# Performance work log

Measured on AMD Instinct MI355X. Metric: run time of the kernel, lower is better.

## Reference

```python
import jax, jax.numpy as jnp
import numpy as np

B, T, HID = 2, 1024, 768
EXPAND, NH, HD, NG, NS, K = 2, 24, 64, 1, 128, 4
INTER = EXPAND * HID            # 1536
CONV_DIM = INTER + 2 * NG * NS  # 1792
NLVL = 15                       # get_num_levels(16384, base=2)
EPS = 1e-5


def _levels(T):
    # Fenwick-style hierarchical level matrix (HType.WEAK, base 2):
    # level(t, s) = 0 on the diagonal, else msb(t XOR s) + 1.
    t = np.arange(T)
    x = t[:, None] ^ t[None, :]
    lev = np.zeros((T, T), np.int32)
    nz = x > 0
    lev[nz] = np.floor(np.log2(x[nz])).astype(np.int32) + 1
    return lev

_LEV = jnp.asarray(_levels(T))  # [T,T] int32, values in [0, NLVL)


def setup_inputs() -> dict:
    key = jax.random.key(0)
    ks = jax.random.split(key, 4)
    P = INTER + CONV_DIM + NH * (NLVL + 1)  # 3712
    return {
        "hidden_states": jax.random.normal(ks[0], (B, T, HID), jnp.float32),
        "in_proj_w": jax.random.normal(ks[1], (P, HID), jnp.float32) * (HID ** -0.5),
        "conv_w": jax.random.normal(ks[2], (CONV_DIM, 1, K), jnp.float32) * 0.2,
        "conv_b": jnp.zeros((CONV_DIM,), jnp.float32),
        "dt_bias": jnp.ones((NH,), jnp.float32),
        "A_log": jnp.log(jnp.arange(1, NH + 1, dtype=jnp.float32)),
        "L": jnp.ones((NH, NLVL), jnp.float32),
        "D": jnp.ones((NH,), jnp.float32),
        "norm_weight": jnp.ones((INTER,), jnp.float32),
        "out_proj_w": jax.random.normal(ks[3], (HID, INTER), jnp.float32) * (INTER ** -0.5),
    }


def reference(hidden_states, in_proj_w, conv_w, conv_b, dt_bias, A_log, L, D,
              norm_weight, out_proj_w):
    # in_proj and split: [gate | xBC | dt | dl]
    proj = hidden_states @ in_proj_w.T                       # [B,T,P]
    gate = proj[..., :INTER]
    xBC = proj[..., INTER:INTER + CONV_DIM]
    dt = proj[..., INTER + CONV_DIM:INTER + CONV_DIM + NH]
    dl = proj[..., INTER + CONV_DIM + NH:].reshape(B, T, NH, NLVL)

    # fused causal depthwise conv1d + SiLU
    xBC = jax.lax.conv_general_dilated(
        xBC.transpose(0, 2, 1), conv_w, window_strides=(1,),
        padding=[(K - 1, 0)], dimension_numbers=("NCH", "OIH", "NCH"),
        feature_group_count=CONV_DIM) + conv_b[None, :, None]
    xBC = jax.nn.silu(xBC.transpose(0, 2, 1))                # [B,T,CONV_DIM]

    x = xBC[..., :INTER].reshape(B, T, NH, HD)               # [B,T,H,P]
    Bm = xBC[..., INTER:INTER + NG * NS].reshape(B, T, NG, NS)
    Cm = xBC[..., INTER + NG * NS:].reshape(B, T, NG, NS)
    hpg = NH // NG
    Bh = jnp.repeat(Bm, hpg, axis=2)                         # [B,T,H,N]
    Ch = jnp.repeat(Cm, hpg, axis=2)

    dt = jax.nn.softplus(dt + dt_bias)                       # [B,T,H]
    A = -jnp.exp(A_log)                                      # [H]
    cumA = jnp.cumsum(dt * A, axis=1)                        # [B,T,H]

    # semiseparable decay exp(sum_{s<r<=t} dt_r * A), causal-masked
    cA = cumA.transpose(0, 2, 1)                             # [B,H,T]
    diff = cA[:, :, :, None] - cA[:, :, None, :]             # [B,H,T,T]
    mask = jnp.tril(jnp.ones((T, T), bool))
    decay = jnp.exp(jnp.where(mask[None, None], diff, -1e9))

    CB = jnp.einsum("bthn,bshn->bhts", Ch, Bh)               # [B,H,T,T]

    # hierarchical lambda gating: positive lambda, per-head learned scale L
    lam = jax.nn.softplus(dl) * L                            # [B,T,H,NLVL]
    lam_g = jnp.take_along_axis(lam.transpose(0, 2, 1, 3),
                                _LEV[None, None], axis=-1)   # [B,H,T,T]

    M = CB * decay * lam_g * dt.transpose(0, 2, 1)[:, :, None, :]
    y = jnp.einsum("bhts,bshp->bthp", M, x)                  # [B,T,H,P]
    y = y + D[None, None, :, None] * x
    y = y.reshape(B, T, INTER)

    # gated RMSNorm (norm_before_gate=False): norm(y * silu(gate))
    y = y * jax.nn.silu(gate)
    var = jnp.mean(jnp.square(y), axis=-1, keepdims=True)
    y = y * jax.lax.rsqrt(var + EPS) * norm_weight

    return y @ out_proj_w.T                                  # [B,T,HID]
```

## Files before the change

### kernel.cpp

```cpp
#include <hip/hip_runtime.h>
#include <hip/hip_bf16.h>
#include <math.h>

#define B_ 2
#define T_ 1024
#define HID_ 768
#define INTER_ 1536
#define NH_ 24
#define HD_ 64
#define NS_ 128
#define NLVL_ 15
#define CONV_DIM_ 1792
#define P_ 3712
#define EPS_ 1e-5f

typedef short short8_t __attribute__((ext_vector_type(8)));
typedef short short4_t __attribute__((ext_vector_type(4)));
typedef float float4_t __attribute__((ext_vector_type(4)));


__device__ __forceinline__ float softplus_f(float x) {
  return (x > 20.f) ? x : log1pf(__expf(x));
}
__device__ __forceinline__ short f2bf(float f) {
  union { float f; unsigned u; } v; v.f = f;
  unsigned r = v.u + 0x7FFF + ((v.u >> 16) & 1);
  return (short)(r >> 16);
}
__device__ __forceinline__ float bf2f(short s) {
  union { unsigned u; float f; } v; v.u = ((unsigned)(unsigned short)s) << 16;
  return v.f;
}
__device__ __forceinline__ void gl_lds16(const void* g, void* l) {
  __builtin_amdgcn_global_load_lds(
      (const __attribute__((address_space(1))) unsigned int*)g,
      (__attribute__((address_space(3))) unsigned int*)l, 16, 0, 0);
}

__global__ __launch_bounds__(256) void cvtdt_k(
    const float* __restrict__ hs, const float* __restrict__ Win, const float* __restrict__ Wout,
    short* __restrict__ hsbf, short* __restrict__ wibf, short* __restrict__ wobf,
    float* __restrict__ dtraw, int ncvt)
{
  const long na = (long)B_ * T_ * HID_, nb = (long)P_ * HID_, nc = (long)HID_ * INTER_;
  if ((int)blockIdx.x < ncvt) {
    const long i = ((long)blockIdx.x * 256 + threadIdx.x) * 8;
    const float* src; short* dst; long off;
    if (i < na)           { src = hs;   dst = hsbf; off = i; }
    else if (i < na + nb) { src = Win;  dst = wibf; off = i - na; }
    else if (i < na + nb + nc) { src = Wout; dst = wobf; off = i - na - nb; }
    else return;
    const long base = (off & ~31L) + ((off >> 3) & 3) * 4;
    float4 v0 = *(const float4*)(src + base);
    float4 v1 = *(const float4*)(src + base + 16);
    short8_t o;
    o[0] = f2bf(v0.x); o[1] = f2bf(v0.y); o[2] = f2bf(v0.z); o[3] = f2bf(v0.w);
    o[4] = f2bf(v1.x); o[5] = f2bf(v1.y); o[6] = f2bf(v1.z); o[7] = f2bf(v1.w);
    *(short8_t*)(dst + off) = o;
  } else {
    const int rowbt = ((int)blockIdx.x - ncvt) * 4 + (threadIdx.x >> 6);
    const int lane = threadIdx.x & 63;
    float hv[12];
    const float* hrow = hs + (long)rowbt * HID_ + lane * 12;
    #pragma unroll
    for (int j = 0; j < 12; j++) hv[j] = hrow[j];
    const float* wbase = Win + (long)(INTER_ + CONV_DIM_) * HID_ + lane * 12;
    for (int h = 0; h < NH_; h++) {
      const float* wr = wbase + (long)h * HID_;
      float s = 0.f;
      #pragma unroll
      for (int j = 0; j < 12; j++) s = fmaf(hv[j], wr[j], s);
      #pragma unroll
      for (int off = 32; off; off >>= 1) s += __shfl_xor(s, off);
      if (lane == 0) dtraw[(long)rowbt * NH_ + h] = s;
    }
  }
}

__device__ __forceinline__ short8_t ldfrag(const short* Ts, int row, int lg) {
  return *(const short8_t*)(Ts + row * 32 + lg * 8);
}

__device__ __forceinline__ short8_t ldfrag64(const short* Ts, int row, int kk, int lg) {
  const int cc = (kk * 4 + lg) ^ (row & 7);
  return *(const short8_t*)(Ts + row * 64 + cc * 8);
}

__global__ __launch_bounds__(256) void inproj_scan_k(
    const short* __restrict__ A, const short* __restrict__ B, short* __restrict__ C,
    const float* __restrict__ dtraw, const float* __restrict__ dt_bias,
    const float* __restrict__ A_log, float* __restrict__ dtT, float* __restrict__ cAT,
    float* __restrict__ qT)
{
  constexpr int TM = 128, TN = 128, K = HID_;
  constexpr int ASZ = TM * 32, BSZ = TN * 32;
  __shared__ short As[2 * ASZ];
  __shared__ short Bs[2 * BSZ];

  if (blockIdx.y >= 16) {
    const int sid = ((int)blockIdx.y - 16) * 29 + (int)blockIdx.x;
    if (sid >= B_ * NH_) return;
    const int b = sid / NH_;
    const int h = sid % NH_;
    const float bias = dt_bias[h];
    const float Ah = -__expf(A_log[h]);
    const long ob = (long)(h * B_ + b) * T_;
    float* sc = (float*)As;
    float carry = 0.f;
    for (int c0 = 0; c0 < T_; c0 += 256) {
      const int t = c0 + threadIdx.x;
      const long bt = (long)b * T_ + t;
      float sp = softplus_f(dtraw[bt * NH_ + h] + bias);
      dtT[ob + t] = sp;
      sc[threadIdx.x] = sp * Ah;
      __syncthreads();
      for (int off = 1; off < 256; off <<= 1) {
        float add = (threadIdx.x >= off) ? sc[threadIdx.x - off] : 0.f;
        __syncthreads();
        sc[threadIdx.x] += add;
        __syncthreads();
      }
      cAT[ob + t] = carry + sc[threadIdx.x];
      qT[ob + t] = sp * __expf(sc[threadIdx.x | 63] - sc[threadIdx.x]);
      float tot = sc[255];
      __syncthreads();
      carry += tot;
    }
    return;
  }

  const int tid = threadIdx.x;
  const int w = tid >> 6, lane = tid & 63;
  const int lr = lane & 15, lg = lane >> 4;
  const int wr = w >> 1, wc = w & 1;
  const int m0 = blockIdx.y * TM, n0 = blockIdx.x * TN;
  const int srow = lane >> 2;
  const int sc2 = (lane & 3) * 8;

  auto stage = [&](int buf, int k0) {
    #pragma unroll
    for (int it = 0; it < TM / 64; it++) {
      const int cb = w + 4 * it;
      const int row = cb * 16 + srow;
      gl_lds16(A + (long)(m0 + row) * K + k0 + sc2, As + buf * ASZ + cb * 512);
    }
    #pragma unroll
    for (int it = 0; it < TN / 64; it++) {
      const int cb = w + 4 * it;
      const int row = cb * 16 + srow;
      gl_lds16(B + (long)(n0 + row) * K + k0 + sc2, Bs + buf * BSZ + cb * 512);
    }
  };

  float4_t acc[4][4] = {};
  int cur = 0;
  stage(0, 0);
  for (int k0 = 0; k0 < K; k0 += 32) {
    __syncthreads();
    if (k0 + 32 < K) stage(cur ^ 1, k0 + 32);
    const short* Ab = As + cur * ASZ;
    const short* Bb = Bs + cur * BSZ;
    short8_t af[4], bf[4];
    #pragma unroll
    for (int m = 0; m < 4; m++) af[m] = ldfrag(Ab, wr * 64 + m * 16 + lr, lg);
    #pragma unroll
    for (int n = 0; n < 4; n++) bf[n] = ldfrag(Bb, wc * 64 + n * 16 + lr, lg);
    #pragma unroll
    for (int m = 0; m < 4; m++)
      #pragma unroll
      for (int n = 0; n < 4; n++)
        acc[m][n] = __builtin_amdgcn_mfma_f32_16x16x32_bf16(af[m], bf[n], acc[m][n], 0, 0, 0);
    cur ^= 1;
  }

  #pragma unroll
  for (int m = 0; m < 4; m++)
    #pragma unroll
    for (int n = 0; n < 4; n++)
      #pragma unroll
      for (int r = 0; r < 4; r++) {
        const int row = m0 + wr * 64 + m * 16 + lg * 4 + r;
        const int col = n0 + wc * 64 + n * 16 + lr;
        C[(long)row * P_ + col] = f2bf(acc[m][n][r]);
      }
}

__global__ __launch_bounds__(256) void gemm_out_k(
    const short* __restrict__ A, const short* __restrict__ B, float* __restrict__ C,
    int M, int N, int K)
{
  constexpr int PSZ = 64 * 32;
  constexpr int BKG = 4;
  constexpr int BUF = PSZ * BKG;
  __shared__ short As[2 * BUF];
  __shared__ short Bs[2 * BUF];
  const int tid = threadIdx.x;
  const int w = tid >> 6, lane = tid & 63;
  const int lr = lane & 15, lg = lane >> 4;
  const int wr = w >> 1, wc = w & 1;
  const int m0 = blockIdx.y * 64, n0 = blockIdx.x * 64;
  const int srow = lane >> 2;
  const int sc = (lane & 3) * 8;

  auto stage = [&](int buf, int k0) {
    const int row = w * 16 + srow;
    #pragma unroll
    for (int kg = 0; kg < BKG; kg++) {
      gl_lds16(A + (long)(m0 + row) * K + k0 + kg * 32 + sc, As + buf * BUF + kg * PSZ + w * 512);
      gl_lds16(B + (long)(n0 + row) * K + k0 + kg * 32 + sc, Bs + buf * BUF + kg * PSZ + w * 512);
    }
  };

  float4_t acc[2][2] = {};
  int cur = 0;
  stage(0, 0);
  for (int k0 = 0; k0 < K; k0 += 128) {
    __syncthreads();
    if (k0 + 128 < K) stage(cur ^ 1, k0 + 128);
    #pragma unroll
    for (int kg = 0; kg < BKG; kg++) {
      const short* Ab = As + cur * BUF + kg * PSZ;
      const short* Bb = Bs + cur * BUF + kg * PSZ;
      short8_t af[2], bf[2];
      #pragma unroll
      for (int m = 0; m < 2; m++) af[m] = ldfrag(Ab, wr * 32 + m * 16 + lr, lg);
      #pragma unroll
      for (int n = 0; n < 2; n++) bf[n] = ldfrag(Bb, wc * 32 + n * 16 + lr, lg);
      #pragma unroll
      for (int m = 0; m < 2; m++)
        #pragma unroll
        for (int n = 0; n < 2; n++)
          acc[m][n] = __builtin_amdgcn_mfma_f32_16x16x32_bf16(af[m], bf[n], acc[m][n], 0, 0, 0);
    }
    cur ^= 1;
  }

  #pragma unroll
  for (int m = 0; m < 2; m++)
    #pragma unroll
    for (int n = 0; n < 2; n++)
      #pragma unroll
      for (int r = 0; r < 4; r++) {
        const int row = m0 + wr * 32 + m * 16 + lg * 4 + r;
        const int col = n0 + wc * 32 + n * 16 + lr;
        C[(long)row * N + col] = acc[m][n][r];
      }
}

__global__ __launch_bounds__(256) void gemm_cbh_k(
    const short* __restrict__ Chh, const short* __restrict__ Bh, short* __restrict__ CBh)
{
  if (blockIdx.x > blockIdx.y) return;
  Chh += (long)blockIdx.z * T_ * NS_;
  Bh  += (long)blockIdx.z * T_ * NS_;
  CBh += (long)blockIdx.z * T_ * T_;
  constexpr int PSZ = 64 * 32;
  __shared__ short As[4 * PSZ];
  __shared__ short Bs[4 * PSZ];
  const int tid = threadIdx.x;
  const int w = tid >> 6, lane = tid & 63;
  const int lr = lane & 15, lg = lane >> 4;
  const int wr = w >> 1, wc = w & 1;
  const int m0 = blockIdx.y * 64, n0 = blockIdx.x * 64;
  const int srow = lane >> 2;
  const int sc = (lane & 3) * 8;

  {
    const int row = w * 16 + srow;
    #pragma unroll
    for (int kg = 0; kg < 4; kg++) {
      gl_lds16(Chh + (long)(m0 + row) * NS_ + kg * 32 + sc, As + kg * PSZ + w * 512);
      gl_lds16(Bh  + (long)(n0 + row) * NS_ + kg * 32 + sc, Bs + kg * PSZ + w * 512);
    }
  }
  __syncthreads();

  float4_t acc[2][2] = {};
  #pragma unroll
  for (int kg = 0; kg < 4; kg++) {
    const short* Ab = As + kg * PSZ;
    const short* Bb = Bs + kg * PSZ;
    short8_t af[2], bf[2];
    #pragma unroll
    for (int m = 0; m < 2; m++) af[m] = ldfrag(Ab, wr * 32 + m * 16 + lr, lg);
    #pragma unroll
    for (int n = 0; n < 2; n++) bf[n] = ldfrag(Bb, wc * 32 + n * 16 + lr, lg);
    #pragma unroll
    for (int m = 0; m < 2; m++)
      #pragma unroll
      for (int n = 0; n < 2; n++)
        acc[m][n] = __builtin_amdgcn_mfma_f32_16x16x32_bf16(af[m], bf[n], acc[m][n], 0, 0, 0);
  }

  #pragma unroll
  for (int m = 0; m < 2; m++)
    #pragma unroll
    for (int n = 0; n < 2; n++)
      #pragma unroll
      for (int r = 0; r < 4; r++) {
        const int row = m0 + wr * 32 + m * 16 + lg * 4 + r;
        const int sl = wc * 32 + n * 16 + lr;
        const int g = sl >> 5, k32 = sl & 31;
        const int cc = g * 4 + ((k32 >> 2) & 3);
        const int off = ((cc ^ (row & 7)) * 8) + 4 * (k32 >> 4) + (k32 & 3);
        CBh[(long)row * T_ + n0 + off] = f2bf(acc[m][n][r]);
      }
}

__global__ __launch_bounds__(256) void conv_silu_k(
    const short* __restrict__ projh, const float* __restrict__ cw, const float* __restrict__ cbias,
    const float* __restrict__ qT,
    short* __restrict__ xbf, short* __restrict__ xTr, short* __restrict__ xTq,
    short* __restrict__ Bh, short* __restrict__ Chh)
{
  const int c0 = blockIdx.x * 256;
  const int t0 = blockIdx.y * 16;
  const int b  = blockIdx.z;
  const int tid = threadIdx.x;
  __shared__ float S[19][256];
  #pragma unroll
  for (int r = 0; r < 19; r++) {
    const int t = t0 - 3 + r;
    S[r][tid] = (t >= 0) ? bf2f(projh[((long)b * T_ + t) * P_ + INTER_ + c0 + tid]) : 0.f;
  }
  __syncthreads();
  const int c = c0 + tid;
  const float4 w = *(const float4*)(cw + c * 4);
  const float bias = cbias[c];
  float acc[16];
  #pragma unroll
  for (int tt = 0; tt < 16; tt++) {
    float a = bias + w.w * S[tt + 3][tid] + w.z * S[tt + 2][tid]
                   + w.y * S[tt + 1][tid] + w.x * S[tt][tid];
    acc[tt] = a / (1.f + __expf(-a));
  }
  if (c < INTER_) {
    const int h = c >> 6, hd = c & 63;
    #pragma unroll
    for (int tt = 0; tt < 16; tt++)
      xbf[((long)b * T_ + t0 + tt) * INTER_ + c] = f2bf(acc[tt]);
    const long chb = (long)(h * B_ + b) * T_;
    float qv[16];
    #pragma unroll
    for (int qq = 0; qq < 4; qq++) {
      float4 q4 = *(const float4*)(qT + chb + t0 + qq * 4);
      qv[qq*4+0] = q4.x; qv[qq*4+1] = q4.y; qv[qq*4+2] = q4.z; qv[qq*4+3] = q4.w;
    }
    const long base = ((long)(b * NH_ + h) * HD_ + hd) * T_ + (t0 & ~63);
    const int g = (t0 >> 5) & 1, h2 = (t0 >> 4) & 1, sw = hd & 7;
    #pragma unroll
    for (int a = 0; a < 4; a++) {
      short4_t xr, xq;
      #pragma unroll
      for (int r = 0; r < 4; r++) {
        xr[r] = f2bf(acc[a * 4 + r]);
        xq[r] = f2bf(acc[a * 4 + r] * qv[a * 4 + r]);
      }
      const int off = (((g * 4 + a) ^ sw) * 8) + h2 * 4;
      *(short4_t*)(xTr + base + off) = xr;
      *(short4_t*)(xTq + base + off) = xq;
    }
  } else {
    const int ch0 = c - INTER_;
    const bool isB = ch0 < NS_;
    const int k = isB ? ch0 : ch0 - NS_;
    const int k32 = k & 31;
    const int P = (k & ~31) + 8 * ((k32 >> 2) & 3) + 4 * (k32 >> 4) + (k32 & 3);
    short* dst = isB ? Bh : Chh;
    #pragma unroll
    for (int tt = 0; tt < 16; tt++) {
      const long bt = (long)b * T_ + t0 + tt;
      dst[bt * NS_ + P] = f2bf(acc[tt]);
    }
  }
}

__global__ __launch_bounds__(256) void attn_mfma3_k(
    const short* __restrict__ xTr, const short* __restrict__ xTq,
    const short* __restrict__ CBh,
    const float* __restrict__ cAT, const float* __restrict__ dtT,
    const short* __restrict__ projh, const float* __restrict__ Lw,
    short* __restrict__ ybh)
{
  const int h = blockIdx.x;
  const int tt = (T_ / 64 - 1) - blockIdx.y;
  const int b = blockIdx.z;
  const int t0 = tt * 64;
  const int tid = threadIdx.x;
  const int w = tid >> 6, lane = tid & 63;
  const int lr = lane & 15, lg = lane >> 4;

  __shared__ short CBl[2][64 * 64];
  __shared__ short Xl[2][64 * 64];
  __shared__ float lamS[64][17];

  for (int f = tid; f < 64 * NLVL_; f += 256) {
    int r = f / NLVL_, l = f - r * NLVL_;
    lamS[r][l] = softplus_f(
        bf2f(projh[((long)b * T_ + t0 + r) * P_ + INTER_ + CONV_DIM_ + NH_ + h * NLVL_ + l]))
        * Lw[h * NLVL_ + l];
  }

  const int tl = w * 16 + lr;
  const int t  = t0 + tl;
  const int orow = w * 16 + lg * 4;
  const long chb = (long)(h * B_ + b) * T_;
  const float catv = cAT[chb + t];
  float cao[4];
  #pragma unroll
  for (int r = 0; r < 4; r++) cao[r] = cAT[chb + t0 + orow + r];

  const short* xbr = xTr + (long)(b * NH_ + h) * HD_ * T_;
  const short* xbq = xTq + (long)(b * NH_ + h) * HD_ * T_;
  const short* CBbase = CBh + (long)b * T_ * T_ + (long)t0 * T_;

  const int srow = w * 16 + (lane >> 3);
  const int sch = (lane & 7) * 8;

  auto stage = [&](int buf, int st) {
    const int s0 = st * 64;
    const short* xsrc = (st == tt) ? xbr : xbq;
    #pragma unroll
    for (int i = 0; i < 2; i++) {
      gl_lds16(CBbase + (long)(srow + i * 8) * T_ + s0 + sch, &CBl[buf][(w * 16 + i * 8) * 64]);
      gl_lds16(xsrc + (long)(srow + i * 8) * T_ + s0 + sch, &Xl[buf][(w * 16 + i * 8) * 64]);
    }
  };

  float4_t acc[4] = {};
  int cur = 0;
  stage(0, 0);
  for (int st = 0; st <= tt; st++) {
    __syncthreads();
    if (st < tt) stage(cur ^ 1, st + 1);
    const int s0 = st * 64;
    if (st < tt) {
      const float caE = cAT[chb + s0 + 63];
      const int lev = 32 - __clz(t0 ^ s0);
      float k1o[4];
      #pragma unroll
      for (int r = 0; r < 4; r++)
        k1o[r] = __expf(cao[r] - caE) * lamS[orow + r][lev];
      float4_t dtile[4] = {};
      __builtin_amdgcn_s_setprio(1);
      #pragma unroll
      for (int kk = 0; kk < 2; kk++) {
        short8_t af = ldfrag64(CBl[cur], tl, kk, lg);
        #pragma unroll
        for (int n = 0; n < 4; n++) {
          short8_t bfv = ldfrag64(Xl[cur], n * 16 + lr, kk, lg);
          dtile[n] = __builtin_amdgcn_mfma_f32_16x16x32_bf16(af, bfv, dtile[n], 0, 0, 0);
        }
      }
      __builtin_amdgcn_s_setprio(0);
      #pragma unroll
      for (int n = 0; n < 4; n++)
        #pragma unroll
        for (int r = 0; r < 4; r++)
          acc[n][r] = fmaf(k1o[r], dtile[n][r], acc[n][r]);
    } else {
      #pragma unroll
      for (int kk = 0; kk < 2; kk++) {
        short8_t cb8 = ldfrag64(CBl[cur], tl, kk, lg);
        short8_t af;
        #pragma unroll
        for (int g = 0; g < 2; g++) {
          const int sb = s0 + kk * 32 + g * 16 + lg * 4;
          float4_t ca4 = *(const float4_t*)(cAT + chb + sb);
          float4_t dt4 = *(const float4_t*)(dtT + chb + sb);
          #pragma unroll
          for (int a = 0; a < 4; a++) {
            const int sg = sb + a;
            float m = 0.f;
            if (sg <= t) {
              const int xo = t ^ sg;
              const int lev2 = xo ? (32 - __clz(xo)) : 0;
              m = bf2f(cb8[g * 4 + a]) * __expf(catv - ca4[a]) * lamS[tl][lev2] * dt4[a];
            }
            af[g * 4 + a] = f2bf(m);
          }
        }
        __builtin_amdgcn_s_setprio(1);
        #pragma unroll
        for (int n = 0; n < 4; n++) {
          short8_t bfv = ldfrag64(Xl[cur], n * 16 + lr, kk, lg);
          acc[n] = __builtin_amdgcn_mfma_f32_16x16x32_bf16(af, bfv, acc[n], 0, 0, 0);
        }
        __builtin_amdgcn_s_setprio(0);
      }
    }
    cur ^= 1;
  }

  #pragma unroll
  for (int n = 0; n < 4; n++) {
    #pragma unroll
    for (int r = 0; r < 4; r++) {
      const int trow = t0 + orow + r;
      const int hd = n * 16 + lr;
      ybh[((long)b * T_ + trow) * INTER_ + h * HD_ + hd] = f2bf(acc[n][r]);
    }
  }
}

__global__ __launch_bounds__(192) void gate_rms_k(
    const short* __restrict__ ybh, const short* __restrict__ projh,
    const short* __restrict__ xbf, const float* __restrict__ Dv,
    const float* __restrict__ nw, short* __restrict__ ynorm)
{
  const long bt = blockIdx.x;
  const short* gp = projh + bt * P_;
  const short* yp = ybh + bt * INTER_;
  const short* xp = xbf + bt * INTER_;
  const int i = threadIdx.x;
  const int lo = (i >> 2) * 32 + (i & 3) * 4;
  const int hi = lo + 16;
  const float Dh = Dv[lo >> 6];
  float v[8];
  float ss = 0.f;
  {
    short4_t g0 = *(const short4_t*)(gp + lo);
    short4_t g1 = *(const short4_t*)(gp + hi);
    short4_t y0 = *(const short4_t*)(yp + lo);
    short4_t y1 = *(const short4_t*)(yp + hi);
    short4_t x0 = *(const short4_t*)(xp + lo);
    short4_t x1 = *(const short4_t*)(xp + hi);
    float ga[8] = {bf2f(g0[0]), bf2f(g0[1]), bf2f(g0[2]), bf2f(g0[3]),
                   bf2f(g1[0]), bf2f(g1[1]), bf2f(g1[2]), bf2f(g1[3])};
    float ya[8] = {bf2f(y0[0]), bf2f(y0[1]), bf2f(y0[2]), bf2f(y0[3]),
                   bf2f(y1[0]), bf2f(y1[1]), bf2f(y1[2]), bf2f(y1[3])};
    float xa[8] = {bf2f(x0[0]), bf2f(x0[1]), bf2f(x0[2]), bf2f(x0[3]),
                   bf2f(x1[0]), bf2f(x1[1]), bf2f(x1[2]), bf2f(x1[3])};
    #pragma unroll
    for (int j = 0; j < 8; j++) {
      float y = ya[j] + Dh * xa[j];
      float val = y * (ga[j] / (1.f + __expf(-ga[j])));
      v[j] = val;
      ss += val * val;
    }
  }
  #pragma unroll
  for (int off = 32; off > 0; off >>= 1) ss += __shfl_xor(ss, off);
  __shared__ float part[3];
  if ((i & 63) == 0) part[i >> 6] = ss;
  __syncthreads();
  const float tot = part[0] + part[1] + part[2];
  const float r = rsqrtf(tot * (1.f / INTER_) + EPS_);
  short8_t o;
  #pragma unroll
  for (int j = 0; j < 8; j++) {
    const int idx = (j < 4) ? (lo + j) : (hi + j - 4);
    o[j] = f2bf(v[j] * r * nw[idx]);
  }
  *(short8_t*)(ynorm + bt * INTER_ + i * 8) = o;
}

extern "C" void kernel_launch(void* const* d_in, const int* in_sizes, int n_in,
                              void* d_out, int out_size, void* d_ws, size_t ws_size,
                              hipStream_t stream) {
  const float* hs   = (const float*)d_in[0];
  const float* Win  = (const float*)d_in[1];
  const float* cw   = (const float*)d_in[2];
  const float* cb   = (const float*)d_in[3];
  const float* dtb  = (const float*)d_in[4];
  const float* Alog = (const float*)d_in[5];
  const float* Lw   = (const float*)d_in[6];
  const float* Dv   = (const float*)d_in[7];
  const float* nw   = (const float*)d_in[8];
  const float* Wout = (const float*)d_in[9];
  float* out = (float*)d_out;

  const long n_hs = (long)B_ * T_ * HID_;
  const long n_wi = (long)P_ * HID_;
  const long n_wo = (long)HID_ * INTER_;

  float* ws = (float*)d_ws;
  long o = 0;
  float* projreg = ws + o; o += (long)B_ * T_ * P_ / 2 + 16;
  short* xbf   = (short*)(ws + o); o += (long)B_ * T_ * INTER_ / 2;
  short* Bh    = (short*)(ws + o); o += (long)B_ * T_ * NS_ / 2;
  short* Chh   = (short*)(ws + o); o += (long)B_ * T_ * NS_ / 2;
  float* dtT   = ws + o; o += (long)B_ * T_ * NH_;
  float* cAT   = ws + o; o += (long)B_ * T_ * NH_;
  float* qT    = ws + o; o += (long)B_ * T_ * NH_;
  float* dtraw = ws + o; o += (long)B_ * T_ * NH_;
  short* CBh   = (short*)(ws + o); o += (long)B_ * T_ * T_ / 2;
  short* ybh   = (short*)(ws + o); o += (long)B_ * T_ * INTER_ / 2;
  float* yxreg = ws + o; o += (long)B_ * T_ * INTER_ / 2;
  short* hsbf  = (short*)(ws + o); o += n_hs / 2;
  short* wibf  = (short*)(ws + o); o += n_wi / 2;
  short* wobf  = (short*)(ws + o); o += n_wo / 2;
  short* projh = (short*)projreg;
  short* xTr   = (short*)yxreg;
  short* ynrmb = (short*)yxreg;
  short* xTq   = hsbf;

  const int ncvt = (int)((n_hs + n_wi + n_wo) / 8 / 256);

  cvtdt_k<<<ncvt + (B_ * T_) / 4, 256, 0, stream>>>(
      hs, Win, Wout, hsbf, wibf, wobf, dtraw, ncvt);
  inproj_scan_k<<<dim3(P_ / 128, 18), 256, 0, stream>>>(
      hsbf, wibf, projh, dtraw, dtb, Alog, dtT, cAT, qT);
  conv_silu_k<<<dim3(CONV_DIM_ / 256, T_ / 16, B_), 256, 0, stream>>>(
      projh, cw, cb, qT, xbf, xTr, xTq, Bh, Chh);
  gemm_cbh_k<<<dim3(T_ / 64, T_ / 64, B_), 256, 0, stream>>>(Chh, Bh, CBh);
  attn_mfma3_k<<<dim3(NH_, T_ / 64, B_), 256, 0, stream>>>(
      xTr, xTq, CBh, cAT, dtT, projh, Lw, ybh);
  gate_rms_k<<<B_ * T_, 192, 0, stream>>>(ybh, projh, xbf, Dv, nw, ynrmb);
  gemm_out_k<<<dim3(HID_ / 64, (B_ * T_) / 64), 256, 0, stream>>>(
      ynrmb, wobf, out, B_ * T_, HID_, INTER_);
}
```

Measured before the change: 110.2 us.

## Fuse D-skip into attention epilogue and deepen in-proj GEMM K-step

```diff
diff --git a/kernel.cpp b/kernel.cpp
--- a/kernel.cpp
+++ b/kernel.cpp
@@ -92,10 +92,11 @@
     const float* __restrict__ A_log, float* __restrict__ dtT, float* __restrict__ cAT,
     float* __restrict__ qT)
 {
-  constexpr int TM = 128, TN = 128, K = HID_;
-  constexpr int ASZ = TM * 32, BSZ = TN * 32;
+  constexpr int TM = 128, TN = 128, K = HID_, BK = 64;
+  constexpr int PSZ = TM * 32;
+  constexpr int ASZ = 2 * PSZ;
   __shared__ short As[2 * ASZ];
-  __shared__ short Bs[2 * BSZ];
+  __shared__ short Bs[2 * ASZ];
 
   if (blockIdx.y >= 16) {
     const int sid = ((int)blockIdx.y - 16) * 29 + (int)blockIdx.x;
@@ -139,37 +140,40 @@
 
   auto stage = [&](int buf, int k0) {
     #pragma unroll
-    for (int it = 0; it < TM / 64; it++) {
+    for (int it = 0; it < 2; it++) {
       const int cb = w + 4 * it;
       const int row = cb * 16 + srow;
-      gl_lds16(A + (long)(m0 + row) * K + k0 + sc2, As + buf * ASZ + cb * 512);
-    }
-    #pragma unroll
-    for (int it = 0; it < TN / 64; it++) {
-      const int cb = w + 4 * it;
-      const int row = cb * 16 + srow;
-      gl_lds16(B + (long)(n0 + row) * K + k0 + sc2, Bs + buf * BSZ + cb * 512);
+      #pragma unroll
+      for (int kg = 0; kg < 2; kg++) {
+        gl_lds16(A + (long)(m0 + row) * K + k0 + kg * 32 + sc2,
+                 As + buf * ASZ + kg * PSZ + cb * 512);
+        gl_lds16(B + (long)(n0 + row) * K + k0 + kg * 32 + sc2,
+                 Bs + buf * ASZ + kg * PSZ + cb * 512);
+      }
     }
   };
 
   float4_t acc[4][4] = {};
   int cur = 0;
   stage(0, 0);
-  for (int k0 = 0; k0 < K; k0 += 32) {
+  for (int k0 = 0; k0 < K; k0 += BK) {
     __syncthreads();
-    if (k0 + 32 < K) stage(cur ^ 1, k0 + 32);
-    const short* Ab = As + cur * ASZ;
-    const short* Bb = Bs + cur * BSZ;
-    short8_t af[4], bf[4];
-    #pragma unroll
-    for (int m = 0; m < 4; m++) af[m] = ldfrag(Ab, wr * 64 + m * 16 + lr, lg);
-    #pragma unroll
-    for (int n = 0; n < 4; n++) bf[n] = ldfrag(Bb, wc * 64 + n * 16 + lr, lg);
-    #pragma unroll
-    for (int m = 0; m < 4; m++)
-      #pragma unroll
-      for (int n = 0; n < 4; n++)
-        acc[m][n] = __builtin_amdgcn_mfma_f32_16x16x32_bf16(af[m], bf[n], acc[m][n], 0, 0, 0);
+    if (k0 + BK < K) stage(cur ^ 1, k0 + BK);
+    #pragma unroll
+    for (int kg = 0; kg < 2; kg++) {
+      const short* Ab = As + cur * ASZ + kg * PSZ;
+      const short* Bb = Bs + cur * ASZ + kg * PSZ;
+      short8_t af[4], bf[4];
+      #pragma unroll
+      for (int m = 0; m < 4; m++) af[m] = ldfrag(Ab, wr * 64 + m * 16 + lr, lg);
+      #pragma unroll
+      for (int n = 0; n < 4; n++) bf[n] = ldfrag(Bb, wc * 64 + n * 16 + lr, lg);
+      #pragma unroll
+      for (int m = 0; m < 4; m++)
+        #pragma unroll
+        for (int n = 0; n < 4; n++)
+          acc[m][n] = __builtin_amdgcn_mfma_f32_16x16x32_bf16(af[m], bf[n], acc[m][n], 0, 0, 0);
+    }
     cur ^= 1;
   }
 
@@ -310,7 +314,7 @@
 __global__ __launch_bounds__(256) void conv_silu_k(
     const short* __restrict__ projh, const float* __restrict__ cw, const float* __restrict__ cbias,
     const float* __restrict__ qT,
-    short* __restrict__ xbf, short* __restrict__ xTr, short* __restrict__ xTq,
+    short* __restrict__ xTr, short* __restrict__ xTq,
     short* __restrict__ Bh, short* __restrict__ Chh)
 {
   const int c0 = blockIdx.x * 256;
@@ -336,9 +340,6 @@
   }
   if (c < INTER_) {
     const int h = c >> 6, hd = c & 63;
-    #pragma unroll
-    for (int tt = 0; tt < 16; tt++)
-      xbf[((long)b * T_ + t0 + tt) * INTER_ + c] = f2bf(acc[tt]);
     const long chb = (long)(h * B_ + b) * T_;
     float qv[16];
     #pragma unroll
@@ -380,6 +381,7 @@
     const short* __restrict__ CBh,
     const float* __restrict__ cAT, const float* __restrict__ dtT,
     const short* __restrict__ projh, const float* __restrict__ Lw,
+    const float* __restrict__ Dv,
     short* __restrict__ ybh)
 {
   const int h = blockIdx.x;
@@ -492,30 +494,31 @@
     cur ^= 1;
   }
 
+  const float Dh = Dv[h];
+  const short* Xd = Xl[cur ^ 1];
   #pragma unroll
   for (int n = 0; n < 4; n++) {
     #pragma unroll
     for (int r = 0; r < 4; r++) {
       const int trow = t0 + orow + r;
       const int hd = n * 16 + lr;
-      ybh[((long)b * T_ + trow) * INTER_ + h * HD_ + hd] = f2bf(acc[n][r]);
+      const int xoff = hd * 64 + ((((w >> 1) * 4 + lg) ^ (hd & 7)) * 8) + (w & 1) * 4 + r;
+      const float xv = bf2f(Xd[xoff]);
+      ybh[((long)b * T_ + trow) * INTER_ + h * HD_ + hd] = f2bf(acc[n][r] + Dh * xv);
     }
   }
 }
 
 __global__ __launch_bounds__(192) void gate_rms_k(
     const short* __restrict__ ybh, const short* __restrict__ projh,
-    const short* __restrict__ xbf, const float* __restrict__ Dv,
     const float* __restrict__ nw, short* __restrict__ ynorm)
 {
   const long bt = blockIdx.x;
   const short* gp = projh + bt * P_;
   const short* yp = ybh + bt * INTER_;
-  const short* xp = xbf + bt * INTER_;
   const int i = threadIdx.x;
   const int lo = (i >> 2) * 32 + (i & 3) * 4;
   const int hi = lo + 16;
-  const float Dh = Dv[lo >> 6];
   float v[8];
   float ss = 0.f;
   {
@@ -523,18 +526,13 @@
     short4_t g1 = *(const short4_t*)(gp + hi);
     short4_t y0 = *(const short4_t*)(yp + lo);
     short4_t y1 = *(const short4_t*)(yp + hi);
-    short4_t x0 = *(const short4_t*)(xp + lo);
-    short4_t x1 = *(const short4_t*)(xp + hi);
     float ga[8] = {bf2f(g0[0]), bf2f(g0[1]), bf2f(g0[2]), bf2f(g0[3]),
                    bf2f(g1[0]), bf2f(g1[1]), bf2f(g1[2]), bf2f(g1[3])};
     float ya[8] = {bf2f(y0[0]), bf2f(y0[1]), bf2f(y0[2]), bf2f(y0[3]),
                    bf2f(y1[0]), bf2f(y1[1]), bf2f(y1[2]), bf2f(y1[3])};
-    float xa[8] = {bf2f(x0[0]), bf2f(x0[1]), bf2f(x0[2]), bf2f(x0[3]),
-                   bf2f(x1[0]), bf2f(x1[1]), bf2f(x1[2]), bf2f(x1[3])};
     #pragma unroll
     for (int j = 0; j < 8; j++) {
-      float y = ya[j] + Dh * xa[j];
-      float val = y * (ga[j] / (1.f + __expf(-ga[j])));
+      float val = ya[j] * (ga[j] / (1.f + __expf(-ga[j])));
       v[j] = val;
       ss += val * val;
     }
@@ -594,6 +592,7 @@
   short* xTr   = (short*)yxreg;
   short* ynrmb = (short*)yxreg;
   short* xTq   = hsbf;
+  (void)xbf;
 
   const int ncvt = (int)((n_hs + n_wi + n_wo) / 8 / 256);
 
@@ -602,11 +601,11 @@
   inproj_scan_k<<<dim3(P_ / 128, 18), 256, 0, stream>>>(
       hsbf, wibf, projh, dtraw, dtb, Alog, dtT, cAT, qT);
   conv_silu_k<<<dim3(CONV_DIM_ / 256, T_ / 16, B_), 256, 0, stream>>>(
-      projh, cw, cb, qT, xbf, xTr, xTq, Bh, Chh);
+      projh, cw, cb, qT, xTr, xTq, Bh, Chh);
   gemm_cbh_k<<<dim3(T_ / 64, T_ / 64, B_), 256, 0, stream>>>(Chh, Bh, CBh);
   attn_mfma3_k<<<dim3(NH_, T_ / 64, B_), 256, 0, stream>>>(
-      xTr, xTq, CBh, cAT, dtT, projh, Lw, ybh);
-  gate_rms_k<<<B_ * T_, 192, 0, stream>>>(ybh, projh, xbf, Dv, nw, ynrmb);
+      xTr, xTq, CBh, cAT, dtT, projh, Lw, Dv, ybh);
+  gate_rms_k<<<B_ * T_, 192, 0, stream>>>(ybh, projh, nw, ynrmb);
   gemm_out_k<<<dim3(HID_ / 64, (B_ * T_) / 64), 256, 0, stream>>>(
       ynrmb, wobf, out, B_ * T_, HID_, INTER_);
 }
```

New measurement: 110.1 us. Within noise of the previous version (-0.1%).
